# Kernel tuning notes

Measured on AMD Instinct MI355X. Metric: run time of the kernel, lower is better.

## Reference

```python
import jax, jax.numpy as jnp
import numpy as np

H = 32  # hidden_size


def gru_layer(x, W_ih, W_hh, b_ih, b_hh):
    """PyTorch-semantics single-layer GRU, batch_first. x: [B,T,I] -> [B,T,H]."""
    # Precompute input projections for all timesteps (one big GEMM).
    gi = jnp.einsum('bti,gi->btg', x, W_ih) + b_ih  # [B,T,3H], gate order r,z,n

    def step(h, gi_t):
        gh = h @ W_hh.T + b_hh                      # [B,3H]
        i_r, i_z, i_n = jnp.split(gi_t, 3, axis=-1)
        h_r, h_z, h_n = jnp.split(gh, 3, axis=-1)
        r = jax.nn.sigmoid(i_r + h_r)
        z = jax.nn.sigmoid(i_z + h_z)
        n = jnp.tanh(i_n + r * h_n)
        h_new = (1.0 - z) * n + z * h
        return h_new, h_new

    h0 = jnp.zeros((x.shape[0], W_hh.shape[1]), x.dtype)
    _, ys = jax.lax.scan(step, h0, jnp.swapaxes(gi, 0, 1))  # scan over T
    return jnp.swapaxes(ys, 0, 1)                            # [B,T,H]


def setup_inputs() -> dict:
    key = jax.random.key(0)
    ks = jax.random.split(key, 13)
    N, C, T = 64, 8, 1024
    s = 0.1
    inp = {"x": jax.random.normal(ks[0], (N, C, T), dtype=jnp.float32)}
    # layer 1: input_size=1; layers 2,3: input_size=H
    inp["W_ih1"] = jax.random.normal(ks[1], (3 * H, 1), dtype=jnp.float32) * s
    inp["W_hh1"] = jax.random.normal(ks[2], (3 * H, H), dtype=jnp.float32) * s
    inp["b_ih1"] = jax.random.normal(ks[3], (3 * H,), dtype=jnp.float32) * s
    inp["b_hh1"] = jax.random.normal(ks[4], (3 * H,), dtype=jnp.float32) * s
    inp["W_ih2"] = jax.random.normal(ks[5], (3 * H, H), dtype=jnp.float32) * s
    inp["W_hh2"] = jax.random.normal(ks[6], (3 * H, H), dtype=jnp.float32) * s
    inp["b_ih2"] = jax.random.normal(ks[7], (3 * H,), dtype=jnp.float32) * s
    inp["b_hh2"] = jax.random.normal(ks[8], (3 * H,), dtype=jnp.float32) * s
    inp["W_ih3"] = jax.random.normal(ks[9], (3 * H, H), dtype=jnp.float32) * s
    inp["W_hh3"] = jax.random.normal(ks[10], (3 * H, H), dtype=jnp.float32) * s
    inp["b_ih3"] = jax.random.normal(ks[11], (3 * H,), dtype=jnp.float32) * s
    inp["b_hh3"] = jax.random.normal(ks[12], (3 * H,), dtype=jnp.float32) * s
    return inp


def reference(x, W_ih1, W_hh1, b_ih1, b_hh1,
              W_ih2, W_hh2, b_ih2, b_hh2,
              W_ih3, W_hh3, b_ih3, b_hh3):
    N, C, T = x.shape
    y = x.reshape(N * C, T, 1)                 # [N*C, T, 1]
    y = gru_layer(y, W_ih1, W_hh1, b_ih1, b_hh1)
    y = gru_layer(y, W_ih2, W_hh2, b_ih2, b_hh2)
    y = gru_layer(y, W_ih3, W_hh3, b_ih3, b_hh3)  # [N*C, T, H]
    # Faithful to original (including its permute-then-view layout scramble):
    out = jnp.transpose(y, (1, 0, 2)).reshape(N, C, T, H)
    return out
```

## Files before the change

kernel.cpp:

```cpp
#include <hip/hip_runtime.h>

#define TT 1024
#define HH 32

__device__ __forceinline__ float fast_sigmoid(float x) {
    float e = __builtin_amdgcn_exp2f(x * -1.4426950408889634f);
    return __builtin_amdgcn_rcpf(1.0f + e);
}
__device__ __forceinline__ float fast_tanh(float x) {
    float e = __builtin_amdgcn_exp2f(x * -2.8853900817779268f);
    return fmaf(2.0f, __builtin_amdgcn_rcpf(1.0f + e), -1.0f);
}

__device__ __forceinline__ void acc3(const float4 w0, const float4 w1, const float4 w2,
                                     const float4 v, float4& a0, float4& a1, float4& a2) {
    a0.x = fmaf(w0.x, v.x, a0.x); a0.y = fmaf(w0.y, v.y, a0.y);
    a0.z = fmaf(w0.z, v.z, a0.z); a0.w = fmaf(w0.w, v.w, a0.w);
    a1.x = fmaf(w1.x, v.x, a1.x); a1.y = fmaf(w1.y, v.y, a1.y);
    a1.z = fmaf(w1.z, v.z, a1.z); a1.w = fmaf(w1.w, v.w, a1.w);
    a2.x = fmaf(w2.x, v.x, a2.x); a2.y = fmaf(w2.y, v.y, a2.y);
    a2.z = fmaf(w2.z, v.z, a2.z); a2.w = fmaf(w2.w, v.w, a2.w);
}
__device__ __forceinline__ float hsum(const float4 a) {
    return (a.x + a.y) + (a.z + a.w);
}

__global__ __launch_bounds__(192) void gru3_fused(
    const float* __restrict__ x,
    const float* __restrict__ Wih1, const float* __restrict__ Whh1,
    const float* __restrict__ bih1, const float* __restrict__ bhh1,
    const float* __restrict__ Wih2, const float* __restrict__ Whh2,
    const float* __restrict__ bih2, const float* __restrict__ bhh2,
    const float* __restrict__ Wih3, const float* __restrict__ Whh3,
    const float* __restrict__ bih3, const float* __restrict__ bhh3,
    float* __restrict__ out)
{
    __shared__ float ybuf[3 * 2 * 32];
    __shared__ float xs[TT];

    const int tid  = threadIdx.x;
    const int wid  = tid >> 6;
    const int lane = tid & 63;
    const int h    = lane & 31;
    const int kh   = lane >> 5;
    const int k0   = kh * 16;
    const int bb   = (int)blockIdx.x;

    if (tid < 192) ybuf[tid] = 0.0f;
    {
        const float4* xr4 = (const float4*)(x + bb * TT);
        for (int j = tid; j < TT / 4; j += 192) ((float4*)xs)[j] = xr4[j];
    }

    const float* Whh = (wid == 0) ? Whh1 : (wid == 1) ? Whh2 : Whh3;
    float4 whh[3][4];
#pragma unroll
    for (int g = 0; g < 3; ++g)
#pragma unroll
        for (int j = 0; j < 4; ++j)
            whh[g][j] = *(const float4*)(Whh + (g * 32 + h) * 32 + k0 + 4 * j);

    float4 wih[3][4];
    float wi_r = 0.f, wi_z = 0.f, wi_n = 0.f;
    if (wid == 0) {
        wi_r = Wih1[h]; wi_z = Wih1[32 + h]; wi_n = Wih1[64 + h];
#pragma unroll
        for (int g = 0; g < 3; ++g)
#pragma unroll
            for (int j = 0; j < 4; ++j)
                wih[g][j] = make_float4(0.f, 0.f, 0.f, 0.f);
    } else {
        const float* Wih = (wid == 1) ? Wih2 : Wih3;
#pragma unroll
        for (int g = 0; g < 3; ++g)
#pragma unroll
            for (int j = 0; j < 4; ++j)
                wih[g][j] = *(const float4*)(Wih + (g * 32 + h) * 32 + k0 + 4 * j);
    }

    const float* bihp = (wid == 0) ? bih1 : (wid == 1) ? bih2 : bih3;
    const float* bhhp = (wid == 0) ? bhh1 : (wid == 1) ? bhh2 : bhh3;
    const float brz_r = bihp[h]      + bhhp[h];
    const float brz_z = bihp[32 + h] + bhhp[32 + h];
    const float b_in  = bihp[64 + h];
    const float b_hn  = bhhp[64 + h];

    __syncthreads();

    float hprev = 0.0f;
    for (int i = 0; i < TT + 2; ++i) {
        const int t = i - wid;
        if (t >= 0 && t < TT) {
            const int p = t & 1;

            const float4* vop = (const float4*)(ybuf + wid * 64 + (p ^ 1) * 32 + k0);
            const float4 vo0 = vop[0], vo1 = vop[1], vo2 = vop[2], vo3 = vop[3];

            float4 a0 = make_float4(0.f, 0.f, 0.f, 0.f), a1 = a0, a2 = a0;
            acc3(whh[0][0], whh[1][0], whh[2][0], vo0, a0, a1, a2);
            acc3(whh[0][1], whh[1][1], whh[2][1], vo1, a0, a1, a2);
            acc3(whh[0][2], whh[1][2], whh[2][2], vo2, a0, a1, a2);
            acc3(whh[0][3], whh[1][3], whh[2][3], vo3, a0, a1, a2);
            float shr = hsum(a0), shz = hsum(a1), shn = hsum(a2);

            float pir, piz, pin;
            if (wid == 0) {
                const float xv = xs[t];
                pir = xv * wi_r; piz = xv * wi_z; pin = xv * wi_n;
            } else {
                const float4* vip = (const float4*)(ybuf + (wid - 1) * 64 + p * 32 + k0);
                const float4 vi0 = vip[0], vi1 = vip[1], vi2 = vip[2], vi3 = vip[3];
                float4 b0 = make_float4(0.f, 0.f, 0.f, 0.f), b1 = b0, b2 = b0;
                acc3(wih[0][0], wih[1][0], wih[2][0], vi0, b0, b1, b2);
                acc3(wih[0][1], wih[1][1], wih[2][1], vi1, b0, b1, b2);
                acc3(wih[0][2], wih[1][2], wih[2][2], vi2, b0, b1, b2);
                acc3(wih[0][3], wih[1][3], wih[2][3], vi3, b0, b1, b2);
                pir = hsum(b0); piz = hsum(b1); pin = hsum(b2);
                pir += __shfl_xor(pir, 32);
                piz += __shfl_xor(piz, 32);
                pin += __shfl_xor(pin, 32);
            }
            shr += __shfl_xor(shr, 32);
            shz += __shfl_xor(shz, 32);
            shn += __shfl_xor(shn, 32);

            const float r  = fast_sigmoid(pir + shr + brz_r);
            const float z  = fast_sigmoid(piz + shz + brz_z);
            const float n  = fast_tanh(fmaf(r, shn + b_hn, pin + b_in));
            const float hn = fmaf(z, hprev - n, n);
            hprev = hn;

            if (kh == 0) {
                ybuf[wid * 64 + p * 32 + h] = hn;
                if (wid == 2) out[t * 16384 + bb * 32 + h] = hn;
            }
        }
        __syncthreads();
    }
}

extern "C" void kernel_launch(void* const* d_in, const int* in_sizes, int n_in,
                              void* d_out, int out_size, void* d_ws, size_t ws_size,
                              hipStream_t stream) {
    const float* x    = (const float*)d_in[0];
    const float* Wih1 = (const float*)d_in[1];
    const float* Whh1 = (const float*)d_in[2];
    const float* bih1 = (const float*)d_in[3];
    const float* bhh1 = (const float*)d_in[4];
    const float* Wih2 = (const float*)d_in[5];
    const float* Whh2 = (const float*)d_in[6];
    const float* bih2 = (const float*)d_in[7];
    const float* bhh2 = (const float*)d_in[8];
    const float* Wih3 = (const float*)d_in[9];
    const float* Whh3 = (const float*)d_in[10];
    const float* bih3 = (const float*)d_in[11];
    const float* bhh3 = (const float*)d_in[12];

    gru3_fused<<<dim3(512), dim3(192), 0, stream>>>(
        x, Wih1, Whh1, bih1, bhh1,
        Wih2, Whh2, bih2, bhh2,
        Wih3, Whh3, bih3, bhh3,
        (float*)d_out);
}
```

Baseline: 787.1 us.

## Skew GRU layers by 16 steps with ring buffer, sync every 16 steps

Each of the three layer waves now runs 16 timesteps behind the previous one. Hidden states go into a 32-slot shared-memory ring per layer, so a block barrier is needed only once every 16 steps instead of every step. The recurrence inside a layer relies on the fact that one wavefront's shared-memory writes and reads happen in order, so no barrier is needed there. Layer 0 is rearranged so each half-wave computes the full 32-wide dot product without a cross-lane shuffle. The cost is more shared memory and a longer pipeline fill and drain, plus reliance on in-wave memory ordering for correctness.

```diff
diff --git a/kernel.cpp b/kernel.cpp
--- a/kernel.cpp
+++ b/kernel.cpp
@@ -1,7 +1,7 @@
 #include <hip/hip_runtime.h>
 
 #define TT 1024
-#define HH 32
+#define SS 16
 
 __device__ __forceinline__ float fast_sigmoid(float x) {
     float e = __builtin_amdgcn_exp2f(x * -1.4426950408889634f);
@@ -35,7 +35,7 @@
     const float* __restrict__ bih3, const float* __restrict__ bhh3,
     float* __restrict__ out)
 {
-    __shared__ float ybuf[3 * 2 * 32];
+    __shared__ float ybuf[3 * 32 * 64];
     __shared__ float xs[TT];
 
     const int tid  = threadIdx.x;
@@ -46,36 +46,32 @@
     const int k0   = kh * 16;
     const int bb   = (int)blockIdx.x;
 
-    if (tid < 192) ybuf[tid] = 0.0f;
     {
+        float4 z4 = make_float4(0.f, 0.f, 0.f, 0.f);
+        for (int j = tid; j < 1536; j += 192) ((float4*)ybuf)[j] = z4;
         const float4* xr4 = (const float4*)(x + bb * TT);
         for (int j = tid; j < TT / 4; j += 192) ((float4*)xs)[j] = xr4[j];
     }
 
-    const float* Whh = (wid == 0) ? Whh1 : (wid == 1) ? Whh2 : Whh3;
-    float4 whh[3][4];
-#pragma unroll
-    for (int g = 0; g < 3; ++g)
-#pragma unroll
-        for (int j = 0; j < 4; ++j)
-            whh[g][j] = *(const float4*)(Whh + (g * 32 + h) * 32 + k0 + 4 * j);
-
-    float4 wih[3][4];
-    float wi_r = 0.f, wi_z = 0.f, wi_n = 0.f;
+    float4 w[6][4];
     if (wid == 0) {
-        wi_r = Wih1[h]; wi_z = Wih1[32 + h]; wi_n = Wih1[64 + h];
 #pragma unroll
         for (int g = 0; g < 3; ++g)
 #pragma unroll
-            for (int j = 0; j < 4; ++j)
-                wih[g][j] = make_float4(0.f, 0.f, 0.f, 0.f);
+            for (int j = 0; j < 4; ++j) {
+                w[g][j]     = *(const float4*)(Whh1 + (g * 32 + h) * 32 + 4 * j);
+                w[3 + g][j] = *(const float4*)(Whh1 + (g * 32 + h) * 32 + 16 + 4 * j);
+            }
     } else {
+        const float* Whh = (wid == 1) ? Whh2 : Whh3;
         const float* Wih = (wid == 1) ? Wih2 : Wih3;
 #pragma unroll
         for (int g = 0; g < 3; ++g)
 #pragma unroll
-            for (int j = 0; j < 4; ++j)
-                wih[g][j] = *(const float4*)(Wih + (g * 32 + h) * 32 + k0 + 4 * j);
+            for (int j = 0; j < 4; ++j) {
+                w[g][j]     = *(const float4*)(Whh + (g * 32 + h) * 32 + k0 + 4 * j);
+                w[3 + g][j] = *(const float4*)(Wih + (g * 32 + h) * 32 + k0 + 4 * j);
+            }
     }
 
     const float* bihp = (wid == 0) ? bih1 : (wid == 1) ? bih2 : bih3;
@@ -84,58 +80,66 @@
     const float brz_z = bihp[32 + h] + bhhp[32 + h];
     const float b_in  = bihp[64 + h];
     const float b_hn  = bhhp[64 + h];
+    float wi_r = 0.f, wi_z = 0.f, wi_n = 0.f;
+    if (wid == 0) { wi_r = Wih1[h]; wi_z = Wih1[32 + h]; wi_n = Wih1[64 + h]; }
+
+    const int wlane    = kh * 32 + h;
+    const int rlane    = (wid == 0) ? kh * 32 : kh * 32 + k0;
+    const int own_off  = wid * 2048;
+    const int prev_off = (wid - 1) * 2048;
 
     __syncthreads();
 
     float hprev = 0.0f;
-    for (int i = 0; i < TT + 2; ++i) {
-        const int t = i - wid;
+    for (int i = 0; i < TT + 2 * SS; ++i) {
+        const int t = i - (wid << 4);
         if (t >= 0 && t < TT) {
-            const int p = t & 1;
+            const int slot  = t & 31;
+            const int pslot = (t - 1) & 31;
 
-            const float4* vop = (const float4*)(ybuf + wid * 64 + (p ^ 1) * 32 + k0);
-            const float4 vo0 = vop[0], vo1 = vop[1], vo2 = vop[2], vo3 = vop[3];
+            float xv = 0.f;
+            if (wid == 0) xv = xs[t];
 
+            const float* ownp = &ybuf[own_off + pslot * 64 + rlane];
+            const float* inp  = (wid == 0) ? (ownp + 16)
+                                           : &ybuf[prev_off + slot * 64 + rlane];
+            float4 vIn[4], vOwn[4];
+#pragma unroll
+            for (int j = 0; j < 4; ++j) vIn[j]  = ((const float4*)inp)[j];
+#pragma unroll
+            for (int j = 0; j < 4; ++j) vOwn[j] = ((const float4*)ownp)[j];
+
+            float4 b0 = make_float4(0.f, 0.f, 0.f, 0.f), b1 = b0, b2 = b0;
+#pragma unroll
+            for (int j = 0; j < 4; ++j) acc3(w[3][j], w[4][j], w[5][j], vIn[j], b0, b1, b2);
             float4 a0 = make_float4(0.f, 0.f, 0.f, 0.f), a1 = a0, a2 = a0;
-            acc3(whh[0][0], whh[1][0], whh[2][0], vo0, a0, a1, a2);
-            acc3(whh[0][1], whh[1][1], whh[2][1], vo1, a0, a1, a2);
-            acc3(whh[0][2], whh[1][2], whh[2][2], vo2, a0, a1, a2);
-            acc3(whh[0][3], whh[1][3], whh[2][3], vo3, a0, a1, a2);
-            float shr = hsum(a0), shz = hsum(a1), shn = hsum(a2);
+#pragma unroll
+            for (int j = 0; j < 4; ++j) acc3(w[0][j], w[1][j], w[2][j], vOwn[j], a0, a1, a2);
 
-            float pir, piz, pin;
+            const float sr = hsum(a0), sz = hsum(a1), sn = hsum(a2);
+            const float tr = hsum(b0), tz = hsum(b1), tn = hsum(b2);
+
+            float r, z, nn;
             if (wid == 0) {
-                const float xv = xs[t];
-                pir = xv * wi_r; piz = xv * wi_z; pin = xv * wi_n;
+                r  = fast_sigmoid(fmaf(xv, wi_r, sr + tr + brz_r));
+                z  = fast_sigmoid(fmaf(xv, wi_z, sz + tz + brz_z));
+                nn = fast_tanh(fmaf(xv, wi_n, b_in) + r * (sn + tn + b_hn));
             } else {
-                const float4* vip = (const float4*)(ybuf + (wid - 1) * 64 + p * 32 + k0);
-                const float4 vi0 = vip[0], vi1 = vip[1], vi2 = vip[2], vi3 = vip[3];
-                float4 b0 = make_float4(0.f, 0.f, 0.f, 0.f), b1 = b0, b2 = b0;
-                acc3(wih[0][0], wih[1][0], wih[2][0], vi0, b0, b1, b2);
-                acc3(wih[0][1], wih[1][1], wih[2][1], vi1, b0, b1, b2);
-                acc3(wih[0][2], wih[1][2], wih[2][2], vi2, b0, b1, b2);
-                acc3(wih[0][3], wih[1][3], wih[2][3], vi3, b0, b1, b2);
-                pir = hsum(b0); piz = hsum(b1); pin = hsum(b2);
-                pir += __shfl_xor(pir, 32);
-                piz += __shfl_xor(piz, 32);
-                pin += __shfl_xor(pin, 32);
+                float cr = sr + tr;  cr += __shfl_xor(cr, 32);
+                float cz = sz + tz;  cz += __shfl_xor(cz, 32);
+                float ci = tn;       ci += __shfl_xor(ci, 32);
+                float ch = sn;       ch += __shfl_xor(ch, 32);
+                r  = fast_sigmoid(cr + brz_r);
+                z  = fast_sigmoid(cz + brz_z);
+                nn = fast_tanh(ci + b_in + r * (ch + b_hn));
             }
-            shr += __shfl_xor(shr, 32);
-            shz += __shfl_xor(shz, 32);
-            shn += __shfl_xor(shn, 32);
-
-            const float r  = fast_sigmoid(pir + shr + brz_r);
-            const float z  = fast_sigmoid(piz + shz + brz_z);
-            const float n  = fast_tanh(fmaf(r, shn + b_hn, pin + b_in));
-            const float hn = fmaf(z, hprev - n, n);
+            const float hn = fmaf(z, hprev - nn, nn);
             hprev = hn;
-
-            if (kh == 0) {
-                ybuf[wid * 64 + p * 32 + h] = hn;
-                if (wid == 2) out[t * 16384 + bb * 32 + h] = hn;
-            }
+            ybuf[own_off + slot * 64 + wlane] = hn;
+            if (wid == 2 && kh == 0)
+                out[(unsigned)(t * 16384 + bb * 32 + h)] = hn;
         }
-        __syncthreads();
+        if ((i & 15) == 15) __syncthreads();
     }
 }
 
```

Measured after the change: 821.2 us. 4.3% more time.
